# Performance work log

Hardware: AMD Instinct MI355X
Metric: run time of the kernel (lower is better)

Reference implementation:

```python
import jax, jax.numpy as jnp
import numpy as np

NUM_TOPICS = 64
VOCAB_SIZE = 50000
BATCH = 2048
RHO = 0.1

def setup_inputs() -> dict:
    key = jax.random.key(0)
    k_x, k_b, k_t, k_m = jax.random.split(key, 4)
    x = jax.random.uniform(k_x, (BATCH, VOCAB_SIZE), dtype=jnp.float32)  # BoW-like counts
    beta = jax.random.normal(k_b, (NUM_TOPICS, VOCAB_SIZE), dtype=jnp.float32)
    theta = jax.random.normal(k_t, (NUM_TOPICS, NUM_TOPICS), dtype=jnp.float32)
    mu = jax.random.normal(k_m, (NUM_TOPICS,), dtype=jnp.float32)
    return {"x": x, "beta": beta, "theta": theta, "mu": mu}

def reference(x, beta, theta, mu):
    # Original double loop:
    #   log_prob[:,k] = sum(x*beta[k],1) + mu[k] + rho * sum_{j!=k} theta[k,j]*sum(x*beta[j],1)
    # Let s[b,k] = sum_v x[b,v]*beta[k,v] = (x @ beta.T)[b,k].
    # Then log_prob = s + mu + rho * s @ (theta with zeroed diagonal).T
    s = jnp.einsum('bv,kv->bk', x, beta)                      # [B, K]
    theta_off = theta * (1.0 - jnp.eye(theta.shape[0], dtype=theta.dtype))
    log_prob = s + mu[None, :] + RHO * jnp.einsum('bj,kj->bk', s, theta_off)
    return log_prob
```

## Files before the change

kernel.cpp:

```cpp
#include <hip/hip_runtime.h>

typedef unsigned short u16;
typedef unsigned int u32;
typedef unsigned long long u64;

#define VOCAB 50000
#define BATCH 2048
#define NTOP 64
#define RHO 0.1f

#define KSPLIT 32
#define CHUNK 1568
#define NKB 1568
#define GPC 12544
#define KSTEP 128

typedef short bf16x8 __attribute__((ext_vector_type(8)));
typedef float f32x4 __attribute__((ext_vector_type(4)));

__device__ __forceinline__ u16 f32_to_bf16(float f) {
  u32 u = __builtin_bit_cast(u32, f);
  return (u16)((u + 0x8000u) >> 16);
}
__device__ __forceinline__ u32 pack2(float a, float b) {
  return (u32)f32_to_bf16(a) | ((u32)f32_to_bf16(b) << 16);
}
__device__ __forceinline__ u32 cvtpk(float lo, float hi) {
  u32 r;
  asm volatile("v_cvt_pk_bf16_f32 %0, %1, %2" : "=v"(r) : "v"(lo), "v"(hi));
  return r;
}
union frag_cast { u32 w[4]; bf16x8 v; };

__global__ void ctm_prep(const float* __restrict__ beta, u16* __restrict__ bp) {
  int i = blockIdx.x * blockDim.x + threadIdx.x;
  int stride = gridDim.x * blockDim.x;
  for (int j = i; j < NTOP * GPC; j += stride) {
    int col = j / GPC;
    int g = j - col * GPC;
    int k = g * 4;
    float4 v = make_float4(0.f, 0.f, 0.f, 0.f);
    if (k < VOCAB)
      v = *(const float4*)(beta + (u64)col * VOCAB + k);
    int kb = k >> 5;
    int jj = k & 31;
    int pbase = ((jj & 15) >> 2) * 8 + ((jj & 16) ? 4 : 0);
    u32 lo = pack2(v.x, v.y), hi = pack2(v.z, v.w);
    *(uint2*)(bp + (u64)kb * 2048 + col * 32 + pbase) = make_uint2(lo, hi);
  }
}

__global__ void __launch_bounds__(256, 4) ctm_gemm(const float* __restrict__ x,
                                                   const u16* __restrict__ bp,
                                                   float* __restrict__ sp) {
  __shared__ u16 ldsA[64 * KSTEP];
  __shared__ u16 ldsB[4 * 2048];

  const int t = threadIdx.x;
  const int l = t & 63;
  const int w = t >> 6;
  const int fr = l & 15;
  const int fk = l >> 4;

  const int bx = blockIdx.x;
  const int k0 = bx * CHUNK;
  const int kend = (k0 + CHUNK < VOCAB) ? (k0 + CHUNK) : VOCAB;
  const int row0 = blockIdx.y * 64;
  const int nfull = (kend - k0) >> 7;

  const int c = t & 31;
  const int srow = t >> 5;
  const float* xbase = x + (u64)(row0 + srow) * VOCAB + k0 + c * 4;
  const u32 aws = ((u32)(c * 8)) ^ ((u32)srow << 4);

  const u32 bofs = (u32)(w << 12);

  const int arow = w * 16 + fr;
  const u32 arb = (u32)(arow * 256);
  const u32 aswz = (u32)((arow & 7) << 4);

  f32x4 acc[4] = {{0.f,0.f,0.f,0.f},{0.f,0.f,0.f,0.f},{0.f,0.f,0.f,0.f},{0.f,0.f,0.f,0.f}};

  for (int st = 0; st <= nfull; ++st) {
    const int ks0 = k0 + st * KSTEP;
    const int rem = ((kend - ks0) < KSTEP) ? (kend - ks0) : KSTEP;
    if (rem <= 0) break;

    const u64 bsrc = (u64)(ks0 >> 5) * 4096u;
    #pragma unroll
    for (int i = 0; i < 4; ++i) {
      __builtin_amdgcn_global_load_lds(
          (const __attribute__((address_space(1))) void*)
              ((const char*)bp + bsrc + bofs + (u32)(i * 1024) + (u32)(l * 16)),
          (__attribute__((address_space(3))) void*)((char*)ldsB + bofs + (u32)(i * 1024)),
          16, 0, 0);
    }

    if (rem == KSTEP) {
      #pragma unroll
      for (int rr = 0; rr < 8; ++rr) {
        float4 v = *(const float4*)(xbase + (u64)rr * (8 * VOCAB) + st * KSTEP);
        u32 w0 = cvtpk(v.x, v.y), w1 = cvtpk(v.z, v.w);
        *(uint2*)((char*)ldsA + (u32)(srow * 256) + (u32)(rr * 2048) + aws) =
            make_uint2(w0, w1);
      }
    } else {
      #pragma unroll
      for (int rr = 0; rr < 8; ++rr) {
        float4 v = make_float4(0.f, 0.f, 0.f, 0.f);
        if (c * 4 < rem)
          v = *(const float4*)(xbase + (u64)rr * (8 * VOCAB) + st * KSTEP);
        u32 w0 = cvtpk(v.x, v.y), w1 = cvtpk(v.z, v.w);
        *(uint2*)((char*)ldsA + (u32)(srow * 256) + (u32)(rr * 2048) + aws) =
            make_uint2(w0, w1);
      }
    }

    __syncthreads();

    #pragma unroll
    for (int s = 0; s < 4; ++s) {
      const u32 o1 = ((u32)(s * 64 + fk * 8)) ^ aswz;
      const u32 o2 = ((u32)(s * 64 + 32 + fk * 8)) ^ aswz;
      uint2 d1 = *(const uint2*)((const char*)ldsA + arb + o1);
      uint2 d2 = *(const uint2*)((const char*)ldsA + arb + o2);
      frag_cast ua;
      ua.w[0] = d1.x; ua.w[1] = d1.y; ua.w[2] = d2.x; ua.w[3] = d2.y;
      #pragma unroll
      for (int n = 0; n < 4; ++n) {
        bf16x8 bf = *(const bf16x8*)((const char*)ldsB +
                                     (u32)(s * 4096 + (n * 16 + fr) * 64 + fk * 16));
        acc[n] = __builtin_amdgcn_mfma_f32_16x16x32_bf16(ua.v, bf, acc[n], 0, 0, 0);
      }
    }

    __syncthreads();
  }

  float* spb = sp + (u64)bx * (BATCH * NTOP);
  const int orow = row0 + w * 16 + fk * 4;
  #pragma unroll
  for (int n = 0; n < 4; ++n) {
    #pragma unroll
    for (int r = 0; r < 4; ++r)
      spb[(orow + r) * NTOP + ((n << 4) | fr)] = acc[n][r];
  }
}

__global__ void __launch_bounds__(256) ctm_epi(const float* __restrict__ sp,
                                               const float* __restrict__ theta,
                                               const float* __restrict__ mu,
                                               float* __restrict__ out) {
  __shared__ float thT[NTOP * NTOP];
  __shared__ float sb[8 * NTOP];
  const int t = threadIdx.x;
  const int r0 = blockIdx.x * 8;

  #pragma unroll
  for (int i = 0; i < 16; ++i) {
    int e = i * 256 + t;
    thT[(e & 63) * 64 + (e >> 6)] = theta[e];
  }

  const int k = t & 63;
  const int rl = t >> 6;
  #pragma unroll
  for (int rr = 0; rr < 2; ++rr) {
    const int r = rl + rr * 4;
    float sum = 0.f;
    #pragma unroll
    for (int cc = 0; cc < KSPLIT; ++cc)
      sum += sp[(u64)cc * (BATCH * NTOP) + (r0 + r) * NTOP + k];
    sb[r * 64 + k] = sum;
  }
  __syncthreads();

  const float muk = mu[k];
  const float diag = thT[k * 64 + k];
  #pragma unroll
  for (int rr = 0; rr < 2; ++rr) {
    const int r = rl + rr * 4;
    const float* srow = &sb[r * 64];
    float accv = 0.f;
    #pragma unroll 8
    for (int j = 0; j < 64; ++j)
      accv += thT[j * 64 + k] * srow[j];
    const float sv = srow[k];
    out[(r0 + r) * 64 + k] = sv + muk + RHO * (accv - diag * sv);
  }
}

extern "C" void kernel_launch(void* const* d_in, const int* in_sizes, int n_in,
                              void* d_out, int out_size, void* d_ws, size_t ws_size,
                              hipStream_t stream) {
  const float* x = (const float*)d_in[0];
  const float* beta = (const float*)d_in[1];
  const float* theta = (const float*)d_in[2];
  const float* mu = (const float*)d_in[3];
  float* out = (float*)d_out;

  u16* bp = (u16*)d_ws;
  float* sp = (float*)((char*)d_ws + 6422528u);

  ctm_prep<<<1568, 256, 0, stream>>>(beta, bp);
  ctm_gemm<<<dim3(KSPLIT, BATCH / 64), 256, 0, stream>>>(x, bp, sp);
  ctm_epi<<<BATCH / 8, 256, 0, stream>>>(sp, theta, mu, out);
}
```

Baseline: 111.7 us.

## Fuse beta bf16 conversion into GEMM and double-buffer LDS with register prefetch

Drops the separate beta pre-pack kernel. The GEMM now loads fp32 beta directly, converts it to bf16 and writes it into swizzled LDS alongside x. KSTEP drops to 64 and LDS is double-buffered, with the next tile's global loads issued into registers before the MFMA work on the current tile, leaving one barrier per step. This removes a launch and the workspace round-trip for the packed beta. In exchange every row-block reads fp32 beta (twice the bytes, mostly from cache), tiles are smaller and more registers are held live.

```diff
diff --git a/kernel.cpp b/kernel.cpp
--- a/kernel.cpp
+++ b/kernel.cpp
@@ -11,50 +11,24 @@
 
 #define KSPLIT 32
 #define CHUNK 1568
-#define NKB 1568
-#define GPC 12544
-#define KSTEP 128
-
+#define KSTEP 64
+
+typedef short bf16x4 __attribute__((ext_vector_type(4)));
 typedef short bf16x8 __attribute__((ext_vector_type(8)));
 typedef float f32x4 __attribute__((ext_vector_type(4)));
 
-__device__ __forceinline__ u16 f32_to_bf16(float f) {
-  u32 u = __builtin_bit_cast(u32, f);
-  return (u16)((u + 0x8000u) >> 16);
-}
-__device__ __forceinline__ u32 pack2(float a, float b) {
-  return (u32)f32_to_bf16(a) | ((u32)f32_to_bf16(b) << 16);
-}
 __device__ __forceinline__ u32 cvtpk(float lo, float hi) {
   u32 r;
   asm volatile("v_cvt_pk_bf16_f32 %0, %1, %2" : "=v"(r) : "v"(lo), "v"(hi));
   return r;
 }
-union frag_cast { u32 w[4]; bf16x8 v; };
-
-__global__ void ctm_prep(const float* __restrict__ beta, u16* __restrict__ bp) {
-  int i = blockIdx.x * blockDim.x + threadIdx.x;
-  int stride = gridDim.x * blockDim.x;
-  for (int j = i; j < NTOP * GPC; j += stride) {
-    int col = j / GPC;
-    int g = j - col * GPC;
-    int k = g * 4;
-    float4 v = make_float4(0.f, 0.f, 0.f, 0.f);
-    if (k < VOCAB)
-      v = *(const float4*)(beta + (u64)col * VOCAB + k);
-    int kb = k >> 5;
-    int jj = k & 31;
-    int pbase = ((jj & 15) >> 2) * 8 + ((jj & 16) ? 4 : 0);
-    u32 lo = pack2(v.x, v.y), hi = pack2(v.z, v.w);
-    *(uint2*)(bp + (u64)kb * 2048 + col * 32 + pbase) = make_uint2(lo, hi);
-  }
-}
+union frag_cast { bf16x4 h[2]; bf16x8 v; };
 
 __global__ void __launch_bounds__(256, 4) ctm_gemm(const float* __restrict__ x,
-                                                   const u16* __restrict__ bp,
+                                                   const float* __restrict__ beta,
                                                    float* __restrict__ sp) {
-  __shared__ u16 ldsA[64 * KSTEP];
-  __shared__ u16 ldsB[4 * 2048];
+  __shared__ u16 ldsA[2][64 * KSTEP];
+  __shared__ u16 ldsB[2][64 * KSTEP];
 
   const int t = threadIdx.x;
   const int l = t & 63;
@@ -66,75 +40,97 @@
   const int k0 = bx * CHUNK;
   const int kend = (k0 + CHUNK < VOCAB) ? (k0 + CHUNK) : VOCAB;
   const int row0 = blockIdx.y * 64;
-  const int nfull = (kend - k0) >> 7;
-
-  const int c = t & 31;
-  const int srow = t >> 5;
-  const float* xbase = x + (u64)(row0 + srow) * VOCAB + k0 + c * 4;
-  const u32 aws = ((u32)(c * 8)) ^ ((u32)srow << 4);
-
-  const u32 bofs = (u32)(w << 12);
+  const int nsteps = (kend - k0 + KSTEP - 1) >> 6;
+
+  const int c = t & 15;
+  const int srow = t >> 4;
+  const float* xb = x + (u64)(row0 + srow) * VOCAB + k0 + c * 4;
+  const float* betab = beta + (u64)srow * VOCAB + k0 + c * 4;
+  const u32 wofs = (u32)(srow * 128) + (((u32)(c * 8)) ^ ((u32)((srow & 7) << 4)));
 
   const int arow = w * 16 + fr;
-  const u32 arb = (u32)(arow * 256);
+  const u32 arb = (u32)(arow * 128);
   const u32 aswz = (u32)((arow & 7) << 4);
 
   f32x4 acc[4] = {{0.f,0.f,0.f,0.f},{0.f,0.f,0.f,0.f},{0.f,0.f,0.f,0.f},{0.f,0.f,0.f,0.f}};
 
-  for (int st = 0; st <= nfull; ++st) {
-    const int ks0 = k0 + st * KSTEP;
-    const int rem = ((kend - ks0) < KSTEP) ? (kend - ks0) : KSTEP;
-    if (rem <= 0) break;
-
-    const u64 bsrc = (u64)(ks0 >> 5) * 4096u;
+  {
+    const int rem = kend - k0 < KSTEP ? kend - k0 : KSTEP;
+    const bool m = (c * 4) < rem;
+    float4 a0 = make_float4(0,0,0,0), a1 = a0, a2 = a0, a3 = a0;
+    float4 b0 = a0, b1 = a0, b2 = a0, b3 = a0;
+    if (m) {
+      a0 = *(const float4*)(xb);               b0 = *(const float4*)(betab);
+      a1 = *(const float4*)(xb + 16 * VOCAB);  b1 = *(const float4*)(betab + 16 * VOCAB);
+      a2 = *(const float4*)(xb + 32 * VOCAB);  b2 = *(const float4*)(betab + 32 * VOCAB);
+      a3 = *(const float4*)(xb + 48 * VOCAB);  b3 = *(const float4*)(betab + 48 * VOCAB);
+    }
+    *(uint2*)((char*)ldsA[0] + wofs)        = make_uint2(cvtpk(a0.x,a0.y), cvtpk(a0.z,a0.w));
+    *(uint2*)((char*)ldsA[0] + wofs + 2048) = make_uint2(cvtpk(a1.x,a1.y), cvtpk(a1.z,a1.w));
+    *(uint2*)((char*)ldsA[0] + wofs + 4096) = make_uint2(cvtpk(a2.x,a2.y), cvtpk(a2.z,a2.w));
+    *(uint2*)((char*)ldsA[0] + wofs + 6144) = make_uint2(cvtpk(a3.x,a3.y), cvtpk(a3.z,a3.w));
+    *(uint2*)((char*)ldsB[0] + wofs)        = make_uint2(cvtpk(b0.x,b0.y), cvtpk(b0.z,b0.w));
+    *(uint2*)((char*)ldsB[0] + wofs + 2048) = make_uint2(cvtpk(b1.x,b1.y), cvtpk(b1.z,b1.w));
+    *(uint2*)((char*)ldsB[0] + wofs + 4096) = make_uint2(cvtpk(b2.x,b2.y), cvtpk(b2.z,b2.w));
+    *(uint2*)((char*)ldsB[0] + wofs + 6144) = make_uint2(cvtpk(b3.x,b3.y), cvtpk(b3.z,b3.w));
+  }
+  __syncthreads();
+
+  for (int st = 0; st < nsteps; ++st) {
+    const int cb = st & 1;
+    const bool have_next = (st + 1) < nsteps;
+
+    float4 a0, a1, a2, a3, b0, b1, b2, b3;
+    if (have_next) {
+      const int ks = (st + 1) << 6;
+      const int rem = kend - k0 - ks;
+      const bool m = (c * 4) < rem;
+      a0 = a1 = a2 = a3 = make_float4(0,0,0,0);
+      b0 = b1 = b2 = b3 = make_float4(0,0,0,0);
+      if (m) {
+        const float* xp = xb + ks;
+        const float* bp2 = betab + ks;
+        a0 = *(const float4*)(xp);               b0 = *(const float4*)(bp2);
+        a1 = *(const float4*)(xp + 16 * VOCAB);  b1 = *(const float4*)(bp2 + 16 * VOCAB);
+        a2 = *(const float4*)(xp + 32 * VOCAB);  b2 = *(const float4*)(bp2 + 32 * VOCAB);
+        a3 = *(const float4*)(xp + 48 * VOCAB);  b3 = *(const float4*)(bp2 + 48 * VOCAB);
+      }
+    }
+
+    const char* bufA = (const char*)ldsA[cb];
+    const char* bufB = (const char*)ldsB[cb];
     #pragma unroll
-    for (int i = 0; i < 4; ++i) {
-      __builtin_amdgcn_global_load_lds(
-          (const __attribute__((address_space(1))) void*)
-              ((const char*)bp + bsrc + bofs + (u32)(i * 1024) + (u32)(l * 16)),
-          (__attribute__((address_space(3))) void*)((char*)ldsB + bofs + (u32)(i * 1024)),
-          16, 0, 0);
-    }
-
-    if (rem == KSTEP) {
-      #pragma unroll
-      for (int rr = 0; rr < 8; ++rr) {
-        float4 v = *(const float4*)(xbase + (u64)rr * (8 * VOCAB) + st * KSTEP);
-        u32 w0 = cvtpk(v.x, v.y), w1 = cvtpk(v.z, v.w);
-        *(uint2*)((char*)ldsA + (u32)(srow * 256) + (u32)(rr * 2048) + aws) =
-            make_uint2(w0, w1);
-      }
-    } else {
-      #pragma unroll
-      for (int rr = 0; rr < 8; ++rr) {
-        float4 v = make_float4(0.f, 0.f, 0.f, 0.f);
-        if (c * 4 < rem)
-          v = *(const float4*)(xbase + (u64)rr * (8 * VOCAB) + st * KSTEP);
-        u32 w0 = cvtpk(v.x, v.y), w1 = cvtpk(v.z, v.w);
-        *(uint2*)((char*)ldsA + (u32)(srow * 256) + (u32)(rr * 2048) + aws) =
-            make_uint2(w0, w1);
-      }
-    }
-
-    __syncthreads();
-
-    #pragma unroll
-    for (int s = 0; s < 4; ++s) {
-      const u32 o1 = ((u32)(s * 64 + fk * 8)) ^ aswz;
-      const u32 o2 = ((u32)(s * 64 + 32 + fk * 8)) ^ aswz;
-      uint2 d1 = *(const uint2*)((const char*)ldsA + arb + o1);
-      uint2 d2 = *(const uint2*)((const char*)ldsA + arb + o2);
+    for (int s = 0; s < 2; ++s) {
+      const u32 in0 = (u32)(s * 64 + fk * 8);
+      const u32 in1 = in0 + 32;
       frag_cast ua;
-      ua.w[0] = d1.x; ua.w[1] = d1.y; ua.w[2] = d2.x; ua.w[3] = d2.y;
+      ua.h[0] = *(const bf16x4*)(bufA + arb + (in0 ^ aswz));
+      ua.h[1] = *(const bf16x4*)(bufA + arb + (in1 ^ aswz));
       #pragma unroll
       for (int n = 0; n < 4; ++n) {
-        bf16x8 bf = *(const bf16x8*)((const char*)ldsB +
-                                     (u32)(s * 4096 + (n * 16 + fr) * 64 + fk * 16));
-        acc[n] = __builtin_amdgcn_mfma_f32_16x16x32_bf16(ua.v, bf, acc[n], 0, 0, 0);
+        const int bcol = (n << 4) | fr;
+        const u32 brb = (u32)(bcol * 128);
+        const u32 bswz = (u32)((bcol & 7) << 4);
+        frag_cast ub;
+        ub.h[0] = *(const bf16x4*)(bufB + brb + (in0 ^ bswz));
+        ub.h[1] = *(const bf16x4*)(bufB + brb + (in1 ^ bswz));
+        acc[n] = __builtin_amdgcn_mfma_f32_16x16x32_bf16(ua.v, ub.v, acc[n], 0, 0, 0);
       }
     }
 
-    __syncthreads();
+    if (have_next) {
+      char* nA = (char*)ldsA[cb ^ 1];
+      char* nB = (char*)ldsB[cb ^ 1];
+      *(uint2*)(nA + wofs)        = make_uint2(cvtpk(a0.x,a0.y), cvtpk(a0.z,a0.w));
+      *(uint2*)(nA + wofs + 2048) = make_uint2(cvtpk(a1.x,a1.y), cvtpk(a1.z,a1.w));
+      *(uint2*)(nA + wofs + 4096) = make_uint2(cvtpk(a2.x,a2.y), cvtpk(a2.z,a2.w));
+      *(uint2*)(nA + wofs + 6144) = make_uint2(cvtpk(a3.x,a3.y), cvtpk(a3.z,a3.w));
+      *(uint2*)(nB + wofs)        = make_uint2(cvtpk(b0.x,b0.y), cvtpk(b0.z,b0.w));
+      *(uint2*)(nB + wofs + 2048) = make_uint2(cvtpk(b1.x,b1.y), cvtpk(b1.z,b1.w));
+      *(uint2*)(nB + wofs + 4096) = make_uint2(cvtpk(b2.x,b2.y), cvtpk(b2.z,b2.w));
+      *(uint2*)(nB + wofs + 6144) = make_uint2(cvtpk(b3.x,b3.y), cvtpk(b3.z,b3.w));
+      __syncthreads();
+    }
   }
 
   float* spb = sp + (u64)bx * (BATCH * NTOP);
@@ -199,10 +195,8 @@
   const float* mu = (const float*)d_in[3];
   float* out = (float*)d_out;
 
-  u16* bp = (u16*)d_ws;
-  float* sp = (float*)((char*)d_ws + 6422528u);
-
-  ctm_prep<<<1568, 256, 0, stream>>>(beta, bp);
-  ctm_gemm<<<dim3(KSPLIT, BATCH / 64), 256, 0, stream>>>(x, bp, sp);
+  float* sp = (float*)d_ws;
+
+  ctm_gemm<<<dim3(KSPLIT, BATCH / 64), 256, 0, stream>>>(x, beta, sp);
   ctm_epi<<<BATCH / 8, 256, 0, stream>>>(sp, theta, mu, out);
 }
```

After: 109.7 us. Within noise of the previous version (-1.9%).

## Restructure split-K GEMM to 16-row tiles with register-fed B and double-buffered A

Applied to the files above, without the earlier changes.

The GEMM kernel now uses 16-row batch tiles with only 4 K-splits instead of 64-row tiles with 32 K-splits. Each wave reads its beta fragment straight from global memory into registers instead of staging it in LDS. Activation tiles are double-buffered in LDS, with the next step's x loads prefetched into registers, so one barrier per step replaces two. The aim is to cut the partial-sum traffic and epilogue reduction work, and to overlap x loads with MFMA. The cost is that the same beta data is re-read by four times as many row blocks, which raises L2 and global traffic, and each wave has far fewer accumulators.

```diff
diff --git a/kernel.cpp b/kernel.cpp
--- a/kernel.cpp
+++ b/kernel.cpp
@@ -9,12 +9,14 @@
 #define NTOP 64
 #define RHO 0.1f
 
-#define KSPLIT 32
-#define CHUNK 1568
+#define KSPLIT 4
+#define CHUNKA 12512
+#define KSTEP 256
+#define NSTEPS 49
 #define NKB 1568
 #define GPC 12544
-#define KSTEP 128
 
+typedef short bf16x4 __attribute__((ext_vector_type(4)));
 typedef short bf16x8 __attribute__((ext_vector_type(8)));
 typedef float f32x4 __attribute__((ext_vector_type(4)));
 
@@ -30,7 +32,7 @@
   asm volatile("v_cvt_pk_bf16_f32 %0, %1, %2" : "=v"(r) : "v"(lo), "v"(hi));
   return r;
 }
-union frag_cast { u32 w[4]; bf16x8 v; };
+union frag_cast { bf16x4 h[2]; bf16x8 v; };
 
 __global__ void ctm_prep(const float* __restrict__ beta, u16* __restrict__ bp) {
   int i = blockIdx.x * blockDim.x + threadIdx.x;
@@ -50,12 +52,10 @@
   }
 }
 
-__global__ void __launch_bounds__(256, 4) ctm_gemm(const float* __restrict__ x,
+__global__ void __launch_bounds__(256, 2) ctm_gemm(const float* __restrict__ x,
                                                    const u16* __restrict__ bp,
                                                    float* __restrict__ sp) {
-  __shared__ u16 ldsA[64 * KSTEP];
-  __shared__ u16 ldsB[4 * 2048];
-
+  __shared__ u16 ldsA[2][16 * KSTEP];
   const int t = threadIdx.x;
   const int l = t & 63;
   const int w = t >> 6;
@@ -63,88 +63,72 @@
   const int fk = l >> 4;
 
   const int bx = blockIdx.x;
-  const int k0 = bx * CHUNK;
-  const int kend = (k0 + CHUNK < VOCAB) ? (k0 + CHUNK) : VOCAB;
-  const int row0 = blockIdx.y * 64;
-  const int nfull = (kend - k0) >> 7;
+  const int k0 = bx * CHUNKA;
+  const int klen = (k0 + CHUNKA < VOCAB) ? CHUNKA : (VOCAB - k0);
+  const int r0 = blockIdx.y * 16;
 
-  const int c = t & 31;
-  const int srow = t >> 5;
-  const float* xbase = x + (u64)(row0 + srow) * VOCAB + k0 + c * 4;
-  const u32 aws = ((u32)(c * 8)) ^ ((u32)srow << 4);
+  const float* xb = x + (u64)(r0 + w * 4) * VOCAB + k0 + l * 4;
+  u32 wb[4];
+  #pragma unroll
+  for (int j = 0; j < 4; ++j) {
+    const int row = w * 4 + j;
+    wb[j] = (u32)(row * 512) + (((u32)(l * 8)) ^ ((u32)((row & 7) << 4)));
+  }
 
-  const u32 bofs = (u32)(w << 12);
+  const u16* bb = bp + (u64)(k0 >> 5) * 2048 + (w * 16 + fr) * 32 + fk * 8;
 
-  const int arow = w * 16 + fr;
-  const u32 arb = (u32)(arow * 256);
-  const u32 aswz = (u32)((arow & 7) << 4);
+  const u32 arb = (u32)(fr * 512);
+  const u32 aswz = (u32)((fr & 7) << 4);
 
-  f32x4 acc[4] = {{0.f,0.f,0.f,0.f},{0.f,0.f,0.f,0.f},{0.f,0.f,0.f,0.f},{0.f,0.f,0.f,0.f}};
+  f32x4 acc = {0.f, 0.f, 0.f, 0.f};
 
-  for (int st = 0; st <= nfull; ++st) {
-    const int ks0 = k0 + st * KSTEP;
-    const int rem = ((kend - ks0) < KSTEP) ? (kend - ks0) : KSTEP;
-    if (rem <= 0) break;
+  #pragma unroll
+  for (int j = 0; j < 4; ++j) {
+    float4 v = make_float4(0.f, 0.f, 0.f, 0.f);
+    if (l * 4 < klen) v = *(const float4*)(xb + (u64)j * VOCAB);
+    *(uint2*)((char*)ldsA[0] + wb[j]) = make_uint2(cvtpk(v.x, v.y), cvtpk(v.z, v.w));
+  }
+  __syncthreads();
 
-    const u64 bsrc = (u64)(ks0 >> 5) * 4096u;
-    #pragma unroll
-    for (int i = 0; i < 4; ++i) {
-      __builtin_amdgcn_global_load_lds(
-          (const __attribute__((address_space(1))) void*)
-              ((const char*)bp + bsrc + bofs + (u32)(i * 1024) + (u32)(l * 16)),
-          (__attribute__((address_space(3))) void*)((char*)ldsB + bofs + (u32)(i * 1024)),
-          16, 0, 0);
-    }
+  for (int st = 0; st < NSTEPS; ++st) {
+    const int cb = st & 1;
+    const bool have = (st + 1) < NSTEPS;
 
-    if (rem == KSTEP) {
+    float4 av[4];
+    if (have) {
+      const int rem = klen - (st + 1) * KSTEP;
       #pragma unroll
-      for (int rr = 0; rr < 8; ++rr) {
-        float4 v = *(const float4*)(xbase + (u64)rr * (8 * VOCAB) + st * KSTEP);
-        u32 w0 = cvtpk(v.x, v.y), w1 = cvtpk(v.z, v.w);
-        *(uint2*)((char*)ldsA + (u32)(srow * 256) + (u32)(rr * 2048) + aws) =
-            make_uint2(w0, w1);
-      }
-    } else {
-      #pragma unroll
-      for (int rr = 0; rr < 8; ++rr) {
-        float4 v = make_float4(0.f, 0.f, 0.f, 0.f);
-        if (c * 4 < rem)
-          v = *(const float4*)(xbase + (u64)rr * (8 * VOCAB) + st * KSTEP);
-        u32 w0 = cvtpk(v.x, v.y), w1 = cvtpk(v.z, v.w);
-        *(uint2*)((char*)ldsA + (u32)(srow * 256) + (u32)(rr * 2048) + aws) =
-            make_uint2(w0, w1);
+      for (int j = 0; j < 4; ++j) {
+        av[j] = make_float4(0.f, 0.f, 0.f, 0.f);
+        if (l * 4 < rem)
+          av[j] = *(const float4*)(xb + (u64)j * VOCAB + (st + 1) * KSTEP);
       }
     }
 
-    __syncthreads();
-
+    const u16* bs = bb + (u64)st * 8 * 2048;
+    const char* bufA = (const char*)ldsA[cb];
     #pragma unroll
-    for (int s = 0; s < 4; ++s) {
-      const u32 o1 = ((u32)(s * 64 + fk * 8)) ^ aswz;
-      const u32 o2 = ((u32)(s * 64 + 32 + fk * 8)) ^ aswz;
-      uint2 d1 = *(const uint2*)((const char*)ldsA + arb + o1);
-      uint2 d2 = *(const uint2*)((const char*)ldsA + arb + o2);
+    for (int s = 0; s < 8; ++s) {
+      bf16x8 bfr = *(const bf16x8*)(bs + s * 2048);
       frag_cast ua;
-      ua.w[0] = d1.x; ua.w[1] = d1.y; ua.w[2] = d2.x; ua.w[3] = d2.y;
-      #pragma unroll
-      for (int n = 0; n < 4; ++n) {
-        bf16x8 bf = *(const bf16x8*)((const char*)ldsB +
-                                     (u32)(s * 4096 + (n * 16 + fr) * 64 + fk * 16));
-        acc[n] = __builtin_amdgcn_mfma_f32_16x16x32_bf16(ua.v, bf, acc[n], 0, 0, 0);
-      }
+      ua.h[0] = *(const bf16x4*)(bufA + arb + (((u32)(s * 64 + fk * 8)) ^ aswz));
+      ua.h[1] = *(const bf16x4*)(bufA + arb + (((u32)(s * 64 + 32 + fk * 8)) ^ aswz));
+      acc = __builtin_amdgcn_mfma_f32_16x16x32_bf16(ua.v, bfr, acc, 0, 0, 0);
     }
 
-    __syncthreads();
+    if (have) {
+      char* nA = (char*)ldsA[cb ^ 1];
+      #pragma unroll
+      for (int j = 0; j < 4; ++j)
+        *(uint2*)(nA + wb[j]) = make_uint2(cvtpk(av[j].x, av[j].y), cvtpk(av[j].z, av[j].w));
+      __syncthreads();
+    }
   }
 
   float* spb = sp + (u64)bx * (BATCH * NTOP);
-  const int orow = row0 + w * 16 + fk * 4;
   #pragma unroll
-  for (int n = 0; n < 4; ++n) {
-    #pragma unroll
-    for (int r = 0; r < 4; ++r)
-      spb[(orow + r) * NTOP + ((n << 4) | fr)] = acc[n][r];
-  }
+  for (int r = 0; r < 4; ++r)
+    spb[(u64)(r0 + fk * 4 + r) * NTOP + (w * 16 + fr)] = acc[r];
 }
 
 __global__ void __launch_bounds__(256) ctm_epi(const float* __restrict__ sp,
@@ -203,6 +187,6 @@
   float* sp = (float*)((char*)d_ws + 6422528u);
 
   ctm_prep<<<1568, 256, 0, stream>>>(beta, bp);
-  ctm_gemm<<<dim3(KSPLIT, BATCH / 64), 256, 0, stream>>>(x, bp, sp);
+  ctm_gemm<<<dim3(KSPLIT, BATCH / 16), 256, 0, stream>>>(x, bp, sp);
   ctm_epi<<<BATCH / 8, 256, 0, stream>>>(sp, theta, mu, out);
 }
```

Result: slower. 123.1 us (+10.1%).
